# Kernel optimization log

Hardware: AMD Instinct MI355X
Metric: run time of the kernel (lower is better)

The kernel has to match this reference:

```python
import jax, jax.numpy as jnp
import numpy as np

N_NODES = 50000
N_EDGES = 1600000
F_IN = 128
E_DIM = 16
F_HID = 16
K_CHEB = 4
MAX_ELEM = 8
MLP_HID = 4
F_OUT = 8


def setup_inputs() -> dict:
    key = jax.random.key(0)
    ks = jax.random.split(key, 20)
    s = 0.1
    inp = {
        "x": jax.random.normal(ks[0], (N_NODES, F_IN), jnp.float32),
        "edge_index": jax.random.randint(ks[1], (2, N_EDGES), 0, N_NODES),
        "edge_attr": jax.random.normal(ks[2], (N_EDGES, E_DIM), jnp.float32),
        # GATv2Conv params (heads=1)
        "Wl": jax.random.normal(ks[3], (F_IN, F_HID), jnp.float32) * s,
        "bl": jnp.zeros((F_HID,), jnp.float32),
        "Wr": jax.random.normal(ks[4], (F_IN, F_HID), jnp.float32) * s,
        "br": jnp.zeros((F_HID,), jnp.float32),
        "We": jax.random.normal(ks[5], (E_DIM, F_HID), jnp.float32) * s,
        "att": jax.random.normal(ks[6], (F_HID,), jnp.float32) * s,
        "gat_bias": jnp.zeros((F_HID,), jnp.float32),
        # GConvGRU: 6 ChebConvs in order [x_z, h_z, x_r, h_r, x_h, h_h]
        "cheb_W": jax.random.normal(ks[7], (6, K_CHEB, F_HID, F_HID), jnp.float32) * s,
        "cheb_b": jnp.zeros((6, F_HID), jnp.float32),
        # MLPAggregation MLP: 8*16 -> 4 -> 8 (batch-norm at init stats == identity)
        "W1": jax.random.normal(ks[8], (MAX_ELEM * F_HID, MLP_HID), jnp.float32) * s,
        "b1": jnp.zeros((MLP_HID,), jnp.float32),
        "W2": jax.random.normal(ks[9], (MLP_HID, F_OUT), jnp.float32) * s,
        "b2": jnp.zeros((F_OUT,), jnp.float32),
    }
    return inp


def _gatv2(x, src, dst, edge_attr, Wl, bl, Wr, br, We, att, gat_bias):
    N = x.shape[0]
    # add_self_loops with fill_value='mean' on edge_attr (mean of incoming attrs per dst)
    cnt = jax.ops.segment_sum(jnp.ones_like(src, dtype=x.dtype), dst, num_segments=N)
    ea_mean = jax.ops.segment_sum(edge_attr, dst, num_segments=N) / jnp.maximum(cnt, 1.0)[:, None]
    loop = jnp.arange(N)
    src2 = jnp.concatenate([src, loop])
    dst2 = jnp.concatenate([dst, loop])
    ea2 = jnp.concatenate([edge_attr, ea_mean], axis=0)
    xl = x @ Wl + bl          # source transform [N, F_HID]
    xr = x @ Wr + br          # target transform
    em = ea2 @ We             # edge transform   [E+N, F_HID]
    m = xl[src2] + xr[dst2] + em
    alpha = jax.nn.leaky_relu(m, 0.2) @ att  # [E+N]
    amax = jax.ops.segment_max(alpha, dst2, num_segments=N)
    ex = jnp.exp(alpha - amax[dst2])
    denom = jax.ops.segment_sum(ex, dst2, num_segments=N)
    w = ex / (denom[dst2] + 1e-16)
    out = jax.ops.segment_sum(w[:, None] * xl[src2], dst2, num_segments=N)
    return out + gat_bias


def _cheb(x, src, dst, norm, W, b):
    # ChebConv with sym normalization, lambda_max=2 -> scaled Laplacian = -D^-1/2 A D^-1/2
    N = x.shape[0]
    def matvec(v):
        return jax.ops.segment_sum(norm[:, None] * v[src], dst, num_segments=N)
    Tx0 = x
    out = Tx0 @ W[0]
    Tx1 = matvec(Tx0)
    out = out + Tx1 @ W[1]
    for k in range(2, W.shape[0]):
        Tx2 = 2.0 * matvec(Tx1) - Tx0
        out = out + Tx2 @ W[k]
        Tx0, Tx1 = Tx1, Tx2
    return out + b


def reference(x, edge_index, edge_attr, Wl, bl, Wr, br, We, att, gat_bias,
              cheb_W, cheb_b, W1, b1, W2, b2):
    N = x.shape[0]
    src, dst = edge_index[0], edge_index[1]
    # --- GATv2Conv snapshot ---
    h = _gatv2(x, src, dst, edge_attr, Wl, bl, Wr, br, We, att, gat_bias)  # [N,16]
    # --- Chebyshev Laplacian normalization (remove self loops, sym norm) ---
    w = (src != dst).astype(x.dtype)
    deg = jax.ops.segment_sum(w, src, num_segments=N)
    dinv = jnp.where(deg > 0, jax.lax.rsqrt(jnp.maximum(deg, 1e-12)), 0.0)
    norm = -dinv[src] * w * dinv[dst]
    # --- GConvGRU (single step, H0 = 0) ---
    H = jnp.zeros_like(h)
    Z = jax.nn.sigmoid(_cheb(h, src, dst, norm, cheb_W[0], cheb_b[0])
                       + _cheb(H, src, dst, norm, cheb_W[1], cheb_b[1]))
    R = jax.nn.sigmoid(_cheb(h, src, dst, norm, cheb_W[2], cheb_b[2])
                       + _cheb(H, src, dst, norm, cheb_W[3], cheb_b[3]))
    Ht = jnp.tanh(_cheb(h, src, dst, norm, cheb_W[4], cheb_b[4])
                  + _cheb(R * H, src, dst, norm, cheb_W[5], cheb_b[5]))
    H = Z * H + (1.0 - Z) * Ht  # [N,16]
    # --- MLPAggregation with idx = arange(N)+1: each node its own segment ---
    # dense batch [N+1, MAX_ELEM, 16]: segment k>0 holds H[k-1] in slot 0, rest zeros.
    flat = jnp.concatenate([H, jnp.zeros((N, (MAX_ELEM - 1) * F_HID), H.dtype)], axis=1)
    dense = jnp.concatenate([jnp.zeros((1, MAX_ELEM * F_HID), H.dtype), flat], axis=0)
    out = jax.nn.relu(dense @ W1 + b1) @ W2 + b2  # [N+1, 8]
    return out
```

## Files before the change

### kernel.cpp

```cpp
#include <hip/hip_runtime.h>
#include <cmath>


constexpr int N = 50000;
constexpr int E = 1600000;

__global__ __launch_bounds__(256)
void k_node_transform(const float* __restrict__ x,
                      const float* __restrict__ Wl, const float* __restrict__ bl,
                      const float* __restrict__ Wr, const float* __restrict__ br,
                      float* __restrict__ xl, float* __restrict__ xr) {
    __shared__ float sWl[128 * 16];
    __shared__ float sWr[128 * 16];
    int t = threadIdx.x;
    for (int i = t; i < 2048; i += 256) { sWl[i] = Wl[i]; sWr[i] = Wr[i]; }
    __syncthreads();
    int f = t & 15, nl = t >> 4;
    int n = blockIdx.x * 16 + nl;
    const float4* xv = reinterpret_cast<const float4*>(x + (size_t)n * 128);
    float aL = bl[f], aR = br[f];
#pragma unroll 8
    for (int k4 = 0; k4 < 32; ++k4) {
        float4 v = xv[k4];
        int k = k4 * 4;
        aL += v.x * sWl[(k + 0) * 16 + f]; aR += v.x * sWr[(k + 0) * 16 + f];
        aL += v.y * sWl[(k + 1) * 16 + f]; aR += v.y * sWr[(k + 1) * 16 + f];
        aL += v.z * sWl[(k + 2) * 16 + f]; aR += v.z * sWr[(k + 2) * 16 + f];
        aL += v.w * sWl[(k + 3) * 16 + f]; aR += v.w * sWr[(k + 3) * 16 + f];
    }
    xl[n * 16 + f] = aL;
    xr[n * 16 + f] = aR;
}

__global__ __launch_bounds__(256)
void k_hist(const int* __restrict__ ei, int* __restrict__ cnt_in, int* __restrict__ deg_out) {
    int e = blockIdx.x * 256 + threadIdx.x;
    int s = ei[e], d = ei[E + e];
    atomicAdd(&cnt_in[d], 1);
    if (s != d) atomicAdd(&deg_out[s], 1);
}

__global__ __launch_bounds__(1024)
void k_scan(const int* __restrict__ cnt, int* __restrict__ rowptr, int n) {
    __shared__ int ssum[1024];
    int t = threadIdx.x;
    int chunk = (n + 1023) / 1024;
    int lo = t * chunk;
    int hi = lo + chunk; if (hi > n) hi = n; if (lo > n) lo = n;
    int s = 0;
    for (int i = lo; i < hi; ++i) s += cnt[i];
    ssum[t] = s;
    __syncthreads();
    for (int off = 1; off < 1024; off <<= 1) {
        int v = (t >= off) ? ssum[t - off] : 0;
        __syncthreads();
        ssum[t] += v;
        __syncthreads();
    }
    int prefix = (t == 0) ? 0 : ssum[t - 1];
    for (int i = lo; i < hi; ++i) { rowptr[i] = prefix; prefix += cnt[i]; }
    if (t == 0) rowptr[n] = ssum[1023];
}

__global__ __launch_bounds__(256)
void k_edge_alpha(const int* __restrict__ ei, const float* __restrict__ ea,
                  const float* __restrict__ xl, const float* __restrict__ xr,
                  const float* __restrict__ We, const float* __restrict__ att,
                  const int* __restrict__ rowptr, int* __restrict__ ctr,
                  int* __restrict__ ssrc, float* __restrict__ salpha,
                  int* __restrict__ seid) {
    __shared__ float sWe[256];
    __shared__ float satt[16];
    int t = threadIdx.x;
    sWe[t] = We[t];
    if (t < 16) satt[t] = att[t];
    __syncthreads();
    int e = blockIdx.x * 256 + t;
    int s = ei[e], d = ei[E + e];
    const float4* ea4 = reinterpret_cast<const float4*>(ea + (size_t)e * 16);
    float a[16];
#pragma unroll
    for (int j = 0; j < 4; ++j) {
        float4 v = ea4[j];
        a[4 * j] = v.x; a[4 * j + 1] = v.y; a[4 * j + 2] = v.z; a[4 * j + 3] = v.w;
    }
    const float4* xl4 = reinterpret_cast<const float4*>(xl + (size_t)s * 16);
    const float4* xr4 = reinterpret_cast<const float4*>(xr + (size_t)d * 16);
    float xls[16], xrd[16];
#pragma unroll
    for (int j = 0; j < 4; ++j) {
        float4 L = xl4[j], R = xr4[j];
        xls[4 * j] = L.x; xls[4 * j + 1] = L.y; xls[4 * j + 2] = L.z; xls[4 * j + 3] = L.w;
        xrd[4 * j] = R.x; xrd[4 * j + 1] = R.y; xrd[4 * j + 2] = R.z; xrd[4 * j + 3] = R.w;
    }
    float alpha = 0.f;
#pragma unroll
    for (int f = 0; f < 16; ++f) {
        float em = 0.f;
#pragma unroll
        for (int j = 0; j < 16; ++j) em += a[j] * sWe[j * 16 + f];
        float m = xls[f] + xrd[f] + em;
        m = m > 0.f ? m : 0.2f * m;
        alpha += m * satt[f];
    }
    int p = rowptr[d] + atomicAdd(&ctr[d], 1);
    ssrc[p] = s; salpha[p] = alpha; seid[p] = e;
}

__global__ __launch_bounds__(256)
void k_gat(const int* __restrict__ rowptr, const int* __restrict__ ssrc,
           const int* __restrict__ seid, const float* __restrict__ salpha,
           const float* __restrict__ ea, const float* __restrict__ xl,
           const float* __restrict__ xr, const float* __restrict__ We,
           const float* __restrict__ att, const int* __restrict__ deg_out,
           const float* __restrict__ gat_bias,
           const float* __restrict__ Wz0, const float* __restrict__ Wh0,
           float* __restrict__ h, float* __restrict__ hs,
           float* __restrict__ accz, float* __restrict__ acch,
           float* __restrict__ dinv) {
    __shared__ float sWe[256], sWz[256], sWh[256];
    __shared__ float satt[16];
    __shared__ float sbuf[16][17];
    int t = threadIdx.x;
    sWe[t] = We[t]; sWz[t] = Wz0[t]; sWh[t] = Wh0[t];
    if (t < 16) satt[t] = att[t];
    int f = t & 15, nl = t >> 4;
    int n = blockIdx.x * 16 + nl;
    int lo = rowptr[n], hi = rowptr[n + 1];
    float sum = 0.f, amax = -3.0e38f;
    for (int i = lo; i < hi; ++i) {
        sum += ea[(size_t)seid[i] * 16 + f];
        amax = fmaxf(amax, salpha[i]);
    }
    float cnt = (float)(hi - lo);
    sbuf[nl][f] = sum / fmaxf(cnt, 1.f);
    __syncthreads();
    float em = 0.f;
#pragma unroll
    for (int j = 0; j < 16; ++j) em += sbuf[nl][j] * sWe[j * 16 + f];
    float m = xl[n * 16 + f] + xr[n * 16 + f] + em;
    m = m > 0.f ? m : 0.2f * m;
    float c = m * satt[f];
#pragma unroll
    for (int off = 1; off < 16; off <<= 1) c += __shfl_xor(c, off, 64);
    float aloop = c;
    amax = fmaxf(amax, aloop);
    float num = 0.f, den = 0.f;
    for (int i = lo; i < hi; ++i) {
        float ex = expf(salpha[i] - amax);
        int s = ssrc[i];
        num += ex * xl[s * 16 + f];
        den += ex;
    }
    float exl = expf(aloop - amax);
    num += exl * xl[n * 16 + f];
    den += exl;
    float hv = num / (den + 1e-16f) + gat_bias[f];
    float dg = (float)deg_out[n];
    float di = dg > 0.f ? rsqrtf(dg) : 0.f;
    h[n * 16 + f] = hv;
    hs[n * 16 + f] = di * hv;
    if (f == 0) dinv[n] = di;
    __syncthreads();
    sbuf[nl][f] = hv;
    __syncthreads();
    float az = 0.f, ah = 0.f;
#pragma unroll
    for (int j = 0; j < 16; ++j) {
        float v = sbuf[nl][j];
        az += v * sWz[j * 16 + f];
        ah += v * sWh[j * 16 + f];
    }
    accz[n * 16 + f] = az;
    acch[n * 16 + f] = ah;
}

__global__ __launch_bounds__(256)
void k_mvcomb(const int* __restrict__ rowptr, const int* __restrict__ ssrc,
              const float* __restrict__ dinv, const float* __restrict__ Tins,
              const float* __restrict__ Tprev, float* __restrict__ Tstore,
              float* __restrict__ Tscale_store,
              const float* __restrict__ Wzk, const float* __restrict__ Whk,
              float* __restrict__ accz, float* __restrict__ acch, int mode) {
    __shared__ float sWz[256], sWh[256];
    __shared__ float st[16][17];
    int t = threadIdx.x;
    sWz[t] = Wzk[t]; sWh[t] = Whk[t];
    int f = t & 15, nl = t >> 4;
    int n = blockIdx.x * 16 + nl;
    int lo = rowptr[n], hi = rowptr[n + 1];
    float acc = 0.f;
    for (int i = lo; i < hi; ++i) {
        int s = ssrc[i];
        if (s != n) acc += Tins[s * 16 + f];
    }
    float di = dinv[n];
    float tv = -di * acc;
    if (mode) tv = 2.f * tv - Tprev[n * 16 + f];
    if (Tstore)       Tstore[n * 16 + f] = tv;
    if (Tscale_store) Tscale_store[n * 16 + f] = di * tv;
    st[nl][f] = tv;
    __syncthreads();
    float az = accz[n * 16 + f], ah = acch[n * 16 + f];
#pragma unroll
    for (int j = 0; j < 16; ++j) {
        float v = st[nl][j];
        az += v * sWz[j * 16 + f];
        ah += v * sWh[j * 16 + f];
    }
    accz[n * 16 + f] = az;
    acch[n * 16 + f] = ah;
}

__global__ __launch_bounds__(256)
void k_final(const float* __restrict__ accz, const float* __restrict__ acch,
             const float* __restrict__ cheb_b,
             const float* __restrict__ W1, const float* __restrict__ b1,
             const float* __restrict__ W2, const float* __restrict__ b2,
             float* __restrict__ out) {
    int r = blockIdx.x * 256 + threadIdx.x;
    if (r > N) return;
    float H[16];
    if (r == 0) {
#pragma unroll
        for (int j = 0; j < 16; ++j) H[j] = 0.f;
    } else {
        int n = r - 1;
#pragma unroll
        for (int j = 0; j < 16; ++j) {
            float z = accz[n * 16 + j] + cheb_b[0 * 16 + j] + cheb_b[1 * 16 + j];
            z = 1.f / (1.f + expf(-z));
            float ht = tanhf(acch[n * 16 + j] + cheb_b[4 * 16 + j] + cheb_b[5 * 16 + j]);
            H[j] = (1.f - z) * ht;
        }
    }
    float hid[4];
#pragma unroll
    for (int c = 0; c < 4; ++c) {
        float v = b1[c];
#pragma unroll
        for (int j = 0; j < 16; ++j) v += H[j] * W1[j * 4 + c];
        hid[c] = fmaxf(v, 0.f);
    }
#pragma unroll
    for (int o = 0; o < 8; ++o) {
        float v = b2[o];
#pragma unroll
        for (int c = 0; c < 4; ++c) v += hid[c] * W2[c * 8 + o];
        out[(size_t)r * 8 + o] = v;
    }
}

extern "C" void kernel_launch(void* const* d_in, const int* in_sizes, int n_in,
                              void* d_out, int out_size, void* d_ws, size_t ws_size,
                              hipStream_t stream) {
    const float* x    = (const float*)d_in[0];
    const int*   ei   = (const int*)d_in[1];
    const float* ea   = (const float*)d_in[2];
    const float* Wl   = (const float*)d_in[3];
    const float* bl   = (const float*)d_in[4];
    const float* Wr   = (const float*)d_in[5];
    const float* br   = (const float*)d_in[6];
    const float* We   = (const float*)d_in[7];
    const float* att  = (const float*)d_in[8];
    const float* gatb = (const float*)d_in[9];
    const float* chW  = (const float*)d_in[10];
    const float* chb  = (const float*)d_in[11];
    const float* W1   = (const float*)d_in[12];
    const float* b1   = (const float*)d_in[13];
    const float* W2   = (const float*)d_in[14];
    const float* b2   = (const float*)d_in[15];
    float* out = (float*)d_out;

    char* w = (char*)d_ws;
    size_t off = 0;
    auto alloc = [&](size_t elems) {
        off = (off + 15) & ~(size_t)15;
        void* p = w + off;
        off += elems * 4;
        return p;
    };
    int*   cnt_in  = (int*)alloc(N);
    int*   deg_out = (int*)alloc(N);
    int*   ctr     = (int*)alloc(N);
    int*   rowptr  = (int*)alloc(N + 2);
    float* xl      = (float*)alloc(16 * N);
    float* xr      = (float*)alloc(16 * N);
    int*   ssrc    = (int*)alloc(E);
    int*   seid    = (int*)alloc(E);
    float* salpha  = (float*)alloc(E);
    float* dinv    = (float*)alloc(N);
    float* h       = (float*)alloc(16 * N);
    float* hs      = (float*)alloc(16 * N);
    float* accz    = (float*)alloc(16 * N);
    float* acch    = (float*)alloc(16 * N);
    float* T1      = (float*)alloc(16 * N);
    float* Tsa     = (float*)alloc(16 * N);
    float* Tsb     = (float*)alloc(16 * N);
    (void)ws_size; (void)in_sizes; (void)n_in; (void)out_size;

    hipMemsetAsync(cnt_in, 0, (size_t)3 * N * sizeof(int), stream);

    k_node_transform<<<N / 16, 256, 0, stream>>>(x, Wl, bl, Wr, br, xl, xr);
    k_hist<<<E / 256, 256, 0, stream>>>(ei, cnt_in, deg_out);
    k_scan<<<1, 1024, 0, stream>>>(cnt_in, rowptr, N);
    k_edge_alpha<<<E / 256, 256, 0, stream>>>(ei, ea, xl, xr, We, att, rowptr, ctr,
                                              ssrc, salpha, seid);
    k_gat<<<N / 16, 256, 0, stream>>>(rowptr, ssrc, seid, salpha, ea, xl, xr, We, att,
                                      deg_out, gatb, chW + 0 * 256, chW + 16 * 256,
                                      h, hs, accz, acch, dinv);
    k_mvcomb<<<N / 16, 256, 0, stream>>>(rowptr, ssrc, dinv, hs, (const float*)nullptr,
                                         T1, Tsa, chW + 1 * 256, chW + 17 * 256,
                                         accz, acch, 0);
    k_mvcomb<<<N / 16, 256, 0, stream>>>(rowptr, ssrc, dinv, Tsa, h,
                                         (float*)nullptr, Tsb, chW + 2 * 256, chW + 18 * 256,
                                         accz, acch, 1);
    k_mvcomb<<<N / 16, 256, 0, stream>>>(rowptr, ssrc, dinv, Tsb, T1,
                                         (float*)nullptr, (float*)nullptr,
                                         chW + 3 * 256, chW + 19 * 256, accz, acch, 1);
    k_final<<<(N + 1 + 255) / 256, 256, 0, stream>>>(accz, acch, chb, W1, b1, W2, b2, out);
}
```

Baseline: 854.4 us.

## Pack sorted edge data, precompute per-dst edge-embedding sums, fuse final Chebyshev step with MLP

```diff
diff --git a/kernel.cpp b/kernel.cpp
--- a/kernel.cpp
+++ b/kernel.cpp
@@ -44,11 +44,14 @@
 void k_scan(const int* __restrict__ cnt, int* __restrict__ rowptr, int n) {
     __shared__ int ssum[1024];
     int t = threadIdx.x;
-    int chunk = (n + 1023) / 1024;
+    const int chunk = 52;
     int lo = t * chunk;
     int hi = lo + chunk; if (hi > n) hi = n; if (lo > n) lo = n;
     int s = 0;
-    for (int i = lo; i < hi; ++i) s += cnt[i];
+    for (int i = lo; i + 3 < hi; i += 4) {
+        int4 v = *reinterpret_cast<const int4*>(cnt + i);
+        s += v.x + v.y + v.z + v.w;
+    }
     ssum[t] = s;
     __syncthreads();
     for (int off = 1; off < 1024; off <<= 1) {
@@ -67,8 +70,7 @@
                   const float* __restrict__ xl, const float* __restrict__ xr,
                   const float* __restrict__ We, const float* __restrict__ att,
                   const int* __restrict__ rowptr, int* __restrict__ ctr,
-                  int* __restrict__ ssrc, float* __restrict__ salpha,
-                  int* __restrict__ seid) {
+                  int2* __restrict__ sedge, float* __restrict__ emsum) {
     __shared__ float sWe[256];
     __shared__ float satt[16];
     int t = threadIdx.x;
@@ -86,58 +88,59 @@
     }
     const float4* xl4 = reinterpret_cast<const float4*>(xl + (size_t)s * 16);
     const float4* xr4 = reinterpret_cast<const float4*>(xr + (size_t)d * 16);
-    float xls[16], xrd[16];
+    float base[16];
 #pragma unroll
     for (int j = 0; j < 4; ++j) {
         float4 L = xl4[j], R = xr4[j];
-        xls[4 * j] = L.x; xls[4 * j + 1] = L.y; xls[4 * j + 2] = L.z; xls[4 * j + 3] = L.w;
-        xrd[4 * j] = R.x; xrd[4 * j + 1] = R.y; xrd[4 * j + 2] = R.z; xrd[4 * j + 3] = R.w;
-    }
+        base[4 * j]     = L.x + R.x; base[4 * j + 1] = L.y + R.y;
+        base[4 * j + 2] = L.z + R.z; base[4 * j + 3] = L.w + R.w;
+    }
+    float em[16];
     float alpha = 0.f;
 #pragma unroll
     for (int f = 0; f < 16; ++f) {
-        float em = 0.f;
-#pragma unroll
-        for (int j = 0; j < 16; ++j) em += a[j] * sWe[j * 16 + f];
-        float m = xls[f] + xrd[f] + em;
+        float e2 = 0.f;
+#pragma unroll
+        for (int j = 0; j < 16; ++j) e2 += a[j] * sWe[j * 16 + f];
+        em[f] = e2;
+        float m = base[f] + e2;
         m = m > 0.f ? m : 0.2f * m;
         alpha += m * satt[f];
     }
     int p = rowptr[d] + atomicAdd(&ctr[d], 1);
-    ssrc[p] = s; salpha[p] = alpha; seid[p] = e;
-}
-
-__global__ __launch_bounds__(256)
-void k_gat(const int* __restrict__ rowptr, const int* __restrict__ ssrc,
-           const int* __restrict__ seid, const float* __restrict__ salpha,
-           const float* __restrict__ ea, const float* __restrict__ xl,
-           const float* __restrict__ xr, const float* __restrict__ We,
-           const float* __restrict__ att, const int* __restrict__ deg_out,
-           const float* __restrict__ gat_bias,
+    sedge[p] = make_int2(s, __float_as_int(alpha));
+    float* es = emsum + (size_t)d * 16;
+#pragma unroll
+    for (int f = 0; f < 16; ++f) atomicAdd(&es[f], em[f]);
+}
+
+__global__ __launch_bounds__(256)
+void k_gat(const int* __restrict__ rowptr, const int2* __restrict__ sedge,
+           const float* __restrict__ emsum, const float* __restrict__ xl,
+           const float* __restrict__ xr, const int* __restrict__ deg_out,
+           const float* __restrict__ att, const float* __restrict__ gat_bias,
            const float* __restrict__ Wz0, const float* __restrict__ Wh0,
            float* __restrict__ h, float* __restrict__ hs,
            float* __restrict__ accz, float* __restrict__ acch,
            float* __restrict__ dinv) {
-    __shared__ float sWe[256], sWz[256], sWh[256];
+    __shared__ float sWz[256], sWh[256];
     __shared__ float satt[16];
     __shared__ float sbuf[16][17];
     int t = threadIdx.x;
-    sWe[t] = We[t]; sWz[t] = Wz0[t]; sWh[t] = Wh0[t];
+    sWz[t] = Wz0[t]; sWh[t] = Wh0[t];
     if (t < 16) satt[t] = att[t];
+    __syncthreads();
     int f = t & 15, nl = t >> 4;
     int n = blockIdx.x * 16 + nl;
     int lo = rowptr[n], hi = rowptr[n + 1];
-    float sum = 0.f, amax = -3.0e38f;
-    for (int i = lo; i < hi; ++i) {
-        sum += ea[(size_t)seid[i] * 16 + f];
-        amax = fmaxf(amax, salpha[i]);
-    }
+    float amax = -3.0e38f;
+    for (int i = lo + f; i < hi; i += 16)
+        amax = fmaxf(amax, __int_as_float(sedge[i].y));
+#pragma unroll
+    for (int off = 1; off < 16; off <<= 1)
+        amax = fmaxf(amax, __shfl_xor(amax, off, 64));
     float cnt = (float)(hi - lo);
-    sbuf[nl][f] = sum / fmaxf(cnt, 1.f);
-    __syncthreads();
-    float em = 0.f;
-#pragma unroll
-    for (int j = 0; j < 16; ++j) em += sbuf[nl][j] * sWe[j * 16 + f];
+    float em = emsum[(size_t)n * 16 + f] / fmaxf(cnt, 1.f);
     float m = xl[n * 16 + f] + xr[n * 16 + f] + em;
     m = m > 0.f ? m : 0.2f * m;
     float c = m * satt[f];
@@ -147,9 +150,9 @@
     amax = fmaxf(amax, aloop);
     float num = 0.f, den = 0.f;
     for (int i = lo; i < hi; ++i) {
-        float ex = expf(salpha[i] - amax);
-        int s = ssrc[i];
-        num += ex * xl[s * 16 + f];
+        int2 se = sedge[i];
+        float ex = expf(__int_as_float(se.y) - amax);
+        num += ex * xl[se.x * 16 + f];
         den += ex;
     }
     float exl = expf(aloop - amax);
@@ -176,7 +179,7 @@
 }
 
 __global__ __launch_bounds__(256)
-void k_mvcomb(const int* __restrict__ rowptr, const int* __restrict__ ssrc,
+void k_mvcomb(const int* __restrict__ rowptr, const int2* __restrict__ sedge,
               const float* __restrict__ dinv, const float* __restrict__ Tins,
               const float* __restrict__ Tprev, float* __restrict__ Tstore,
               float* __restrict__ Tscale_store,
@@ -191,7 +194,7 @@
     int lo = rowptr[n], hi = rowptr[n + 1];
     float acc = 0.f;
     for (int i = lo; i < hi; ++i) {
-        int s = ssrc[i];
+        int s = sedge[i].x;
         if (s != n) acc += Tins[s * 16 + f];
     }
     float di = dinv[n];
@@ -213,41 +216,69 @@
 }
 
 __global__ __launch_bounds__(256)
-void k_final(const float* __restrict__ accz, const float* __restrict__ acch,
-             const float* __restrict__ cheb_b,
-             const float* __restrict__ W1, const float* __restrict__ b1,
-             const float* __restrict__ W2, const float* __restrict__ b2,
-             float* __restrict__ out) {
-    int r = blockIdx.x * 256 + threadIdx.x;
-    if (r > N) return;
-    float H[16];
-    if (r == 0) {
-#pragma unroll
-        for (int j = 0; j < 16; ++j) H[j] = 0.f;
-    } else {
-        int n = r - 1;
-#pragma unroll
-        for (int j = 0; j < 16; ++j) {
-            float z = accz[n * 16 + j] + cheb_b[0 * 16 + j] + cheb_b[1 * 16 + j];
-            z = 1.f / (1.f + expf(-z));
-            float ht = tanhf(acch[n * 16 + j] + cheb_b[4 * 16 + j] + cheb_b[5 * 16 + j]);
-            H[j] = (1.f - z) * ht;
+void k_mvfinal(const int* __restrict__ rowptr, const int2* __restrict__ sedge,
+               const float* __restrict__ dinv, const float* __restrict__ Tins,
+               const float* __restrict__ Tprev,
+               const float* __restrict__ Wzk, const float* __restrict__ Whk,
+               const float* __restrict__ accz, const float* __restrict__ acch,
+               const float* __restrict__ cheb_b,
+               const float* __restrict__ W1, const float* __restrict__ b1,
+               const float* __restrict__ W2, const float* __restrict__ b2,
+               float* __restrict__ out) {
+    __shared__ float sWz[256], sWh[256];
+    __shared__ float st[16][17];
+    int t = threadIdx.x;
+    sWz[t] = Wzk[t]; sWh[t] = Whk[t];
+    int f = t & 15, nl = t >> 4;
+    int n = blockIdx.x * 16 + nl;
+    int lo = rowptr[n], hi = rowptr[n + 1];
+    float acc = 0.f;
+    for (int i = lo; i < hi; ++i) {
+        int s = sedge[i].x;
+        if (s != n) acc += Tins[s * 16 + f];
+    }
+    float tv = -dinv[n] * acc;
+    tv = 2.f * tv - Tprev[n * 16 + f];
+    st[nl][f] = tv;
+    __syncthreads();
+    float az = accz[n * 16 + f], ah = acch[n * 16 + f];
+#pragma unroll
+    for (int j = 0; j < 16; ++j) {
+        float v = st[nl][j];
+        az += v * sWz[j * 16 + f];
+        ah += v * sWh[j * 16 + f];
+    }
+    float z  = 1.f / (1.f + expf(-(az + cheb_b[f] + cheb_b[16 + f])));
+    float ht = tanhf(ah + cheb_b[64 + f] + cheb_b[80 + f]);
+    float H = (1.f - z) * ht;
+    __syncthreads();
+    st[nl][f] = H;
+    __syncthreads();
+    float hid[4];
+#pragma unroll
+    for (int cc = 0; cc < 4; ++cc) {
+        float v = b1[cc];
+#pragma unroll
+        for (int j = 0; j < 16; ++j) v += st[nl][j] * W1[j * 4 + cc];
+        hid[cc] = fmaxf(v, 0.f);
+    }
+    if (f < 8) {
+        float v = b2[f];
+#pragma unroll
+        for (int cc = 0; cc < 4; ++cc) v += hid[cc] * W2[cc * 8 + f];
+        out[(size_t)(n + 1) * 8 + f] = v;
+    }
+    if (blockIdx.x == 0 && t == 0) {
+        float h0[4];
+#pragma unroll
+        for (int cc = 0; cc < 4; ++cc) h0[cc] = fmaxf(b1[cc], 0.f);
+#pragma unroll
+        for (int o = 0; o < 8; ++o) {
+            float v = b2[o];
+#pragma unroll
+            for (int cc = 0; cc < 4; ++cc) v += h0[cc] * W2[cc * 8 + o];
+            out[o] = v;
         }
-    }
-    float hid[4];
-#pragma unroll
-    for (int c = 0; c < 4; ++c) {
-        float v = b1[c];
-#pragma unroll
-        for (int j = 0; j < 16; ++j) v += H[j] * W1[j * 4 + c];
-        hid[c] = fmaxf(v, 0.f);
-    }
-#pragma unroll
-    for (int o = 0; o < 8; ++o) {
-        float v = b2[o];
-#pragma unroll
-        for (int c = 0; c < 4; ++c) v += hid[c] * W2[c * 8 + o];
-        out[(size_t)r * 8 + o] = v;
     }
 }
 
@@ -283,12 +314,11 @@
     int*   cnt_in  = (int*)alloc(N);
     int*   deg_out = (int*)alloc(N);
     int*   ctr     = (int*)alloc(N);
+    float* emsum   = (float*)alloc(16 * N);
     int*   rowptr  = (int*)alloc(N + 2);
     float* xl      = (float*)alloc(16 * N);
     float* xr      = (float*)alloc(16 * N);
-    int*   ssrc    = (int*)alloc(E);
-    int*   seid    = (int*)alloc(E);
-    float* salpha  = (float*)alloc(E);
+    int2*  sedge   = (int2*)alloc(2 * (size_t)E);
     float* dinv    = (float*)alloc(N);
     float* h       = (float*)alloc(16 * N);
     float* hs      = (float*)alloc(16 * N);
@@ -299,24 +329,23 @@
     float* Tsb     = (float*)alloc(16 * N);
     (void)ws_size; (void)in_sizes; (void)n_in; (void)out_size;
 
-    hipMemsetAsync(cnt_in, 0, (size_t)3 * N * sizeof(int), stream);
+    hipMemsetAsync(cnt_in, 0, (size_t)19 * N * sizeof(int), stream);
 
     k_node_transform<<<N / 16, 256, 0, stream>>>(x, Wl, bl, Wr, br, xl, xr);
     k_hist<<<E / 256, 256, 0, stream>>>(ei, cnt_in, deg_out);
     k_scan<<<1, 1024, 0, stream>>>(cnt_in, rowptr, N);
     k_edge_alpha<<<E / 256, 256, 0, stream>>>(ei, ea, xl, xr, We, att, rowptr, ctr,
-                                              ssrc, salpha, seid);
-    k_gat<<<N / 16, 256, 0, stream>>>(rowptr, ssrc, seid, salpha, ea, xl, xr, We, att,
-                                      deg_out, gatb, chW + 0 * 256, chW + 16 * 256,
+                                              sedge, emsum);
+    k_gat<<<N / 16, 256, 0, stream>>>(rowptr, sedge, emsum, xl, xr, deg_out, att, gatb,
+                                      chW + 0 * 256, chW + 16 * 256,
                                       h, hs, accz, acch, dinv);
-    k_mvcomb<<<N / 16, 256, 0, stream>>>(rowptr, ssrc, dinv, hs, (const float*)nullptr,
+    k_mvcomb<<<N / 16, 256, 0, stream>>>(rowptr, sedge, dinv, hs, (const float*)nullptr,
                                          T1, Tsa, chW + 1 * 256, chW + 17 * 256,
                                          accz, acch, 0);
-    k_mvcomb<<<N / 16, 256, 0, stream>>>(rowptr, ssrc, dinv, Tsa, h,
+    k_mvcomb<<<N / 16, 256, 0, stream>>>(rowptr, sedge, dinv, Tsa, h,
                                          (float*)nullptr, Tsb, chW + 2 * 256, chW + 18 * 256,
                                          accz, acch, 1);
-    k_mvcomb<<<N / 16, 256, 0, stream>>>(rowptr, ssrc, dinv, Tsb, T1,
-                                         (float*)nullptr, (float*)nullptr,
-                                         chW + 3 * 256, chW + 19 * 256, accz, acch, 1);
-    k_final<<<(N + 1 + 255) / 256, 256, 0, stream>>>(accz, acch, chb, W1, b1, W2, b2, out);
-}
+    k_mvfinal<<<N / 16, 256, 0, stream>>>(rowptr, sedge, dinv, Tsb, T1,
+                                          chW + 3 * 256, chW + 19 * 256,
+                                          accz, acch, chb, W1, b1, W2, b2, out);
+}
```

Measured after the change: 1.993 ms. 133% more time.
